# Optimization experiments

Measured on AMD Instinct MI355X. Metric: run time of the kernel, lower is better.

## Reference

```python
import jax, jax.numpy as jnp
import numpy as np

H = 4      # attention heads in HGTConv
DH = 32    # head dim
D = 128    # hidden size (rnn.hidden_size == hidden_size)
PAD = 0    # pad_idx


def setup_inputs() -> dict:
    key = jax.random.key(0)
    ks = jax.random.split(key, 16)
    Na = Np = 50000
    E = 800000
    V = 10000
    L = 8
    s = 0.05  # init scale keeps attention logits stable
    return {
        "tok_author": jax.random.randint(ks[0], (Na, L), 0, V),
        "tok_paper": jax.random.randint(ks[1], (Np, L), 0, V),
        "edge_ap": jax.random.randint(ks[2], (2, E), 0, Np),  # author -> paper
        "edge_pa": jax.random.randint(ks[3], (2, E), 0, Na),  # paper -> author
        "emb": jax.random.normal(ks[4], (V, D)) * s,
        "Wk": jax.random.normal(ks[5], (2, D, D)) * s,
        "Wq": jax.random.normal(ks[6], (2, D, D)) * s,
        "Wv": jax.random.normal(ks[7], (2, D, D)) * s,
        "Watt": jax.random.normal(ks[8], (2, H, DH, DH)) * s,
        "Wmsg": jax.random.normal(ks[9], (2, H, DH, DH)) * s,
        "mu": jnp.ones((2, H), jnp.float32),
        "Wout": jax.random.normal(ks[10], (2, D, D)) * s,
        "lin_w": jax.random.normal(ks[11], (D, D)) * s,
        "lin_b": jnp.zeros((D,), jnp.float32),
    }


def _st_encode(tok, emb):
    # STEncoder stand-in: embedding lookup, pad-masked mean pool, then relu_()
    e = emb[tok]                                   # [N, L, D]
    mask = (tok != PAD).astype(e.dtype)[..., None]  # [N, L, 1]
    pooled = (e * mask).sum(1) / jnp.maximum(mask.sum(1), 1.0)
    return jax.nn.relu(pooled)                     # [N, D]


def _segment_softmax(score, seg, n):
    m = jax.ops.segment_max(score, seg, num_segments=n)
    e = jnp.exp(score - m[seg])
    d = jax.ops.segment_sum(e, seg, num_segments=n)
    return e / (d[seg] + 1e-9)


def _proj(x, W):
    return (x @ W).reshape(x.shape[0], H, DH)


def _rel(k_src, v_src, q_dst, edges, Wa, Wm, mu_r, n_dst):
    # One HGT relation: per-edge key/message transform, segment-softmax attention,
    # scatter-add aggregation into destination nodes.
    src, dst = edges[0], edges[1]
    ke = jnp.einsum('ehd,hdf->ehf', k_src[src], Wa)           # [E, H, DH]
    score = (ke * q_dst[dst]).sum(-1) * mu_r / jnp.sqrt(jnp.float32(DH))  # [E, H]
    alpha = _segment_softmax(score, dst, n_dst)
    me = jnp.einsum('ehd,hdf->ehf', v_src[src], Wm)           # [E, H, DH]
    agg = jax.ops.segment_sum(alpha[..., None] * me, dst, num_segments=n_dst)
    return agg.reshape(n_dst, H * DH)


def reference(tok_author, tok_paper, edge_ap, edge_pa, emb, Wk, Wq, Wv,
              Watt, Wmsg, mu, Wout, lin_w, lin_b):
    # embed + relu per node type
    xa = _st_encode(tok_author, emb)   # [Na, D]
    xp = _st_encode(tok_paper, emb)    # [Np, D]
    Na = xa.shape[0]

    # per-node-type K/Q/V projections (type 0 = author, 1 = paper)
    ka, qa, va = _proj(xa, Wk[0]), _proj(xa, Wq[0]), _proj(xa, Wv[0])
    kp, qp, vp = _proj(xp, Wk[1]), _proj(xp, Wq[1]), _proj(xp, Wv[1])

    # only the 'author' node type feeds the output head, so we only need the
    # paper->author relation's aggregation (rel index 1)
    agg_a = _rel(kp, vp, qa, edge_pa, Watt[1], Wmsg[1], mu[1], Na)
    out_a = jax.nn.gelu(agg_a) @ Wout[0] + xa   # target-type linear + skip

    return out_a @ lin_w + lin_b
```

## Files before the change

kernel.cpp:

```cpp
#include <hip/hip_runtime.h>
#include <math.h>

#define L 8
#define FP8_SCALE 512.0f
#define FP8_INV   0.001953125f

typedef unsigned int  u32;
typedef unsigned short u16;
typedef __attribute__((ext_vector_type(8))) short bf16x8;
typedef __attribute__((ext_vector_type(4))) float f32x4;
typedef __attribute__((ext_vector_type(2))) float f32x2;

__device__ inline u16 f2bf(float x) {
    u32 u = __float_as_uint(x);
    return (u16)((u + 0x7fffu + ((u >> 16) & 1u)) >> 16);
}
__device__ inline float2 bf2f2(u32 v) {
    float2 r;
    r.x = __uint_as_float(v << 16);
    r.y = __uint_as_float(v & 0xffff0000u);
    return r;
}
__device__ inline float gelu_t(float x) {
    return 0.5f * x * (1.0f + tanhf(0.7978845608028654f *
           (x + 0.044715f * x * x * x)));
}

__device__ inline void conv_emb_body(int bid, int tid,
    const float* __restrict__ emb, u32* __restrict__ emb_bf, int n2)
{
    int i = bid * 256 + tid;
    if (i >= n2) return;
    float2 e = *(const float2*)(emb + (size_t)i * 2);
    emb_bf[i] = ((u32)f2bf(e.y) << 16) | (u32)f2bf(e.x);
}

__device__ inline void hist_body8(int bid, int tid,
    const int* __restrict__ dstI, int* __restrict__ deg,
    int* __restrict__ rank, int E, int stride)
{
    int e0 = bid * 256 + tid;
    int d[8], r[8];
#pragma unroll
    for (int j = 0; j < 8; ++j) {
        int e = e0 + j * stride;
        d[j] = (e < E) ? dstI[e] : -1;
    }
#pragma unroll
    for (int j = 0; j < 8; ++j)
        r[j] = (d[j] >= 0) ? atomicAdd(&deg[d[j]], 1) : 0;
#pragma unroll
    for (int j = 0; j < 8; ++j) {
        int e = e0 + j * stride;
        if (d[j] >= 0) rank[e] = r[j];
    }
}

__device__ inline void fold_body(int bid, int tid,
    const float* __restrict__ Wk1, const float* __restrict__ Wq0,
    const float* __restrict__ Wv1, const float* __restrict__ Watt1,
    const float* __restrict__ Wmsg1, const float* __restrict__ Wout0,
    const float* __restrict__ lin_w,
    u16* __restrict__ wkaT, u16* __restrict__ wvmT,
    u16* __restrict__ wqT, u16* __restrict__ w1T, u16* __restrict__ lwT)
{
    int id = bid * 256 + tid;
    int which = id >> 14;
    int idx = id & 16383;
    int col = idx & 127;
    int k = idx >> 7;
    if (which == 0) {
        int h = col >> 5, f = col & 31;
        float s = 0.f;
        for (int d = 0; d < 32; ++d)
            s += Wk1[k * 128 + h * 32 + d] * Watt1[h * 1024 + d * 32 + f];
        wkaT[col * 128 + k] = f2bf(s);
    } else if (which == 1) {
        int h = col >> 5, f = col & 31;
        float s = 0.f;
        for (int d = 0; d < 32; ++d)
            s += Wv1[k * 128 + h * 32 + d] * Wmsg1[h * 1024 + d * 32 + f];
        wvmT[col * 128 + k] = f2bf(s);
    } else if (which == 2) {
        wqT[col * 128 + k] = f2bf(Wq0[k * 128 + col]);
    } else if (which == 3) {
        float s = 0.f;
        for (int d = 0; d < 128; ++d)
            s += Wout0[k * 128 + d] * lin_w[d * 128 + col];
        w1T[col * 128 + k] = f2bf(s);
    } else {
        lwT[col * 128 + k] = f2bf(lin_w[k * 128 + col]);
    }
}

__device__ inline void scan_local_body(int bid, int tid,
    const int* __restrict__ deg, int* __restrict__ locpref,
    int* __restrict__ blocksum, int Na)
{
    __shared__ int lds[256];
    int base = bid * 1024 + tid * 4;
    int4 v = {0, 0, 0, 0};
    if (base + 3 < Na) {
        v = *(const int4*)(deg + base);
    } else {
        if (base + 0 < Na) v.x = deg[base + 0];
        if (base + 1 < Na) v.y = deg[base + 1];
        if (base + 2 < Na) v.z = deg[base + 2];
        if (base + 3 < Na) v.w = deg[base + 3];
    }
    int tot = v.x + v.y + v.z + v.w;
    lds[tid] = tot;
    __syncthreads();
    for (int off = 1; off < 256; off <<= 1) {
        int u = (tid >= off) ? lds[tid - off] : 0;
        __syncthreads();
        lds[tid] += u;
        __syncthreads();
    }
    int excl = lds[tid] - tot;
    if (base < Na) {
        int4 o;
        o.x = excl;
        o.y = excl + v.x;
        o.z = o.y + v.y;
        o.w = o.z + v.z;
        if (base + 3 < Na) *(int4*)(locpref + base) = o;
        else {
            locpref[base] = o.x;
            if (base + 1 < Na) locpref[base + 1] = o.y;
            if (base + 2 < Na) locpref[base + 2] = o.z;
        }
    }
    if (tid == 255) blocksum[bid] = lds[255];
}

__device__ inline void encode_body(int bid, int tid,
    const int* __restrict__ tok_a, const int* __restrict__ tok_p,
    const uint2* __restrict__ emb_bf2,
    uint2* __restrict__ xa2, uint2* __restrict__ xp2, int Na, int Ntot)
{
    int i = bid * 256 + tid;
    int n = i >> 5, q = i & 31;
    if (n >= Ntot) return;
    const int* tok = (n < Na) ? (tok_a + (size_t)n * L)
                              : (tok_p + (size_t)(n - Na) * L);
    int4 t0 = *(const int4*)tok;
    int4 t1 = *(const int4*)(tok + 4);
    int tt[8] = {t0.x, t0.y, t0.z, t0.w, t1.x, t1.y, t1.z, t1.w};
    float ax = 0.f, ay = 0.f, az = 0.f, aw = 0.f;
    int cnt = 0;
#pragma unroll
    for (int l = 0; l < L; ++l) {
        int t = tt[l];
        if (t != 0) {
            cnt++;
            uint2 e = emb_bf2[(size_t)t * 32 + q];
            float2 e0 = bf2f2(e.x), e1 = bf2f2(e.y);
            ax += e0.x; ay += e0.y; az += e1.x; aw += e1.y;
        }
    }
    float dn = 1.0f / fmaxf((float)cnt, 1.0f);
    ax = fmaxf(ax * dn, 0.f); ay = fmaxf(ay * dn, 0.f);
    az = fmaxf(az * dn, 0.f); aw = fmaxf(aw * dn, 0.f);
    uint2 o;
    o.x = ((u32)f2bf(ay) << 16) | (u32)f2bf(ax);
    o.y = ((u32)f2bf(aw) << 16) | (u32)f2bf(az);
    if (n < Na) xa2[(size_t)n * 32 + q] = o;
    else        xp2[(size_t)(n - Na) * 32 + q] = o;
}

__device__ inline void scan_final_body(int bid, int tid,
    const int* __restrict__ locpref, const int* __restrict__ blockoff,
    int* __restrict__ rowptr, int Na)
{
    int i = bid * 256 + tid;
    if (i < Na)
        rowptr[i] = locpref[i] + blockoff[i >> 10];
}

__device__ inline void scatter_body8(int bid, int tid,
    const int* __restrict__ srcI, const int* __restrict__ dstI,
    const int* __restrict__ rank, const int* __restrict__ rowptr,
    int* __restrict__ csrc, int E, int stride)
{
    int e0 = bid * 256 + tid;
    int d[8], s[8], r[8];
#pragma unroll
    for (int j = 0; j < 8; ++j) {
        int e = e0 + j * stride;
        d[j] = (e < E) ? dstI[e] : -1;
        s[j] = (e < E) ? srcI[e] : 0;
        r[j] = (e < E) ? rank[e] : 0;
    }
    int base[8];
#pragma unroll
    for (int j = 0; j < 8; ++j)
        base[j] = (d[j] >= 0) ? rowptr[d[j]] : 0;
#pragma unroll
    for (int j = 0; j < 8; ++j)
        if (d[j] >= 0) csrc[base[j] + r[j]] = s[j];
}

__global__ __launch_bounds__(256) void k_prep(
    const float* emb, u32* emb_bf, int n2,
    const int* dstI, int* deg, int* rank, int E, int Bhist8, int stride,
    const float* Wk1, const float* Wq0, const float* Wv1,
    const float* Watt1, const float* Wmsg1, const float* Wout0,
    const float* lin_w, u16* wkaT, u16* wvmT, u16* wqT, u16* w1T, u16* lwT,
    int Bfold)
{
    int b = blockIdx.x, t = threadIdx.x;
    if (b < Bhist8)               hist_body8(b, t, dstI, deg, rank, E, stride);
    else if (b < Bhist8 + Bfold)  fold_body(b - Bhist8, t, Wk1, Wq0, Wv1,
                                      Watt1, Wmsg1, Wout0, lin_w,
                                      wkaT, wvmT, wqT, w1T, lwT);
    else conv_emb_body(b - Bhist8 - Bfold, t, emb, emb_bf, n2);
}

__global__ __launch_bounds__(256) void k_scan_enc(
    const int* deg, int* locpref, int* blocksum, int Na, int BscanL,
    const int* tok_a, const int* tok_p, const uint2* emb_bf2,
    uint2* xa2, uint2* xp2, int Ntot)
{
    int b = blockIdx.x, t = threadIdx.x;
    if (b < BscanL) scan_local_body(b, t, deg, locpref, blocksum, Na);
    else encode_body(b - BscanL, t, tok_a, tok_p, emb_bf2, xa2, xp2, Na, Ntot);
}

__global__ __launch_bounds__(256) void k_scanb(
    const int* __restrict__ blocksum, int* __restrict__ blockoff,
    int* __restrict__ rowptr, int nb, int Na)
{
    __shared__ int lds[256];
    int t = threadIdx.x;
    int s = (t < nb) ? blocksum[t] : 0;
    lds[t] = s;
    __syncthreads();
    for (int off = 1; off < 256; off <<= 1) {
        int u = (t >= off) ? lds[t - off] : 0;
        __syncthreads();
        lds[t] += u;
        __syncthreads();
    }
    if (t < nb) blockoff[t] = lds[t] - s;
    if (t == 255) rowptr[Na] = lds[255];
}

__global__ __launch_bounds__(256) void k_final(
    const int* locpref, const int* blockoff, int* rowptr, int Na)
{
    scan_final_body(blockIdx.x, threadIdx.x, locpref, blockoff, rowptr, Na);
}

__global__ __launch_bounds__(256) void k_scat_proj(
    const int* srcI, const int* dstI, const int* rank, const int* rowptr,
    int* csrc, int E, int Bscat8, int stride,
    const u16* __restrict__ xa, const u16* __restrict__ xp,
    const u16* __restrict__ wqT, const u16* __restrict__ wkaT,
    const u16* __restrict__ wvmT,
    u16* __restrict__ qa, u32* __restrict__ km8, int Na, int Np, int gba,
    int Bproj)
{
    int b = blockIdx.x, t = threadIdx.x;
    if (b % 3 == 0) {
        int sb = b / 3;
        if (sb < Bscat8)
            scatter_body8(sb, t, srcI, dstI, rank, rowptr, csrc, E, stride);
        return;
    }
    int pb = (b / 3) * 2 + (b % 3 - 1);
    if (pb >= Bproj) return;

    int wave = t >> 6;
    int l = t & 63;
    int x = l & 15;
    int kb = (l >> 4) * 8;

    if (pb < gba) {
        int rbase = pb * 64 + wave * 16;
        int arow = rbase + x;
        if (arow >= Na) arow = Na - 1;
        bf16x8 af[4];
#pragma unroll
        for (int ks = 0; ks < 4; ++ks)
            af[ks] = *(const bf16x8*)(xa + (size_t)arow * 128 + ks * 32 + kb);
        f32x4 acc[8];
#pragma unroll
        for (int ct = 0; ct < 8; ++ct) acc[ct] = (f32x4){0.f, 0.f, 0.f, 0.f};
#pragma unroll
        for (int ks = 0; ks < 4; ++ks)
#pragma unroll
            for (int ct = 0; ct < 8; ++ct) {
                bf16x8 bf = *(const bf16x8*)(wqT + (size_t)(ct * 16 + x) * 128 + ks * 32 + kb);
                acc[ct] = __builtin_amdgcn_mfma_f32_16x16x32_bf16(af[ks], bf, acc[ct], 0, 0, 0);
            }
        int srow = rbase + ((l >> 4) << 2);
#pragma unroll
        for (int ct = 0; ct < 8; ++ct) {
            int col = ct * 16 + x;
#pragma unroll
            for (int r = 0; r < 4; ++r)
                if (srow + r < Na)
                    qa[(size_t)(srow + r) * 128 + col] = f2bf(acc[ct][r]);
        }
    } else {
        int b2 = pb - gba;
        int rbase = b2 * 64 + wave * 16;
        int arow = rbase + x;
        if (arow >= Np) arow = Np - 1;
        bf16x8 af[4];
#pragma unroll
        for (int ks = 0; ks < 4; ++ks)
            af[ks] = *(const bf16x8*)(xp + (size_t)arow * 128 + ks * 32 + kb);
        f32x4 kacc[8], macc[8];
#pragma unroll
        for (int ct = 0; ct < 8; ++ct) {
            kacc[ct] = (f32x4){0.f, 0.f, 0.f, 0.f};
            macc[ct] = (f32x4){0.f, 0.f, 0.f, 0.f};
        }
#pragma unroll
        for (int ks = 0; ks < 4; ++ks)
#pragma unroll
            for (int ct = 0; ct < 8; ++ct) {
                bf16x8 bk = *(const bf16x8*)(wkaT + (size_t)(ct * 16 + x) * 128 + ks * 32 + kb);
                kacc[ct] = __builtin_amdgcn_mfma_f32_16x16x32_bf16(af[ks], bk, kacc[ct], 0, 0, 0);
            }
#pragma unroll
        for (int ks = 0; ks < 4; ++ks)
#pragma unroll
            for (int ct = 0; ct < 8; ++ct) {
                bf16x8 bm = *(const bf16x8*)(wvmT + (size_t)(ct * 16 + x) * 128 + ks * 32 + kb);
                macc[ct] = __builtin_amdgcn_mfma_f32_16x16x32_bf16(af[ks], bm, macc[ct], 0, 0, 0);
            }
        int srow = rbase + ((l >> 4) << 2);
#pragma unroll
        for (int ct = 0; ct < 8; ++ct) {
#pragma unroll
            for (int r = 0; r < 4; ++r) {
                float k0 = kacc[ct][r] * FP8_SCALE;
                float k1 = __shfl_xor(k0, 1);
                float m0 = macc[ct][r] * FP8_SCALE;
                float m1 = __shfl_xor(m0, 1);
                if (!(x & 1) && (srow + r) < Np) {
                    int pk = __builtin_amdgcn_cvt_pk_fp8_f32(k0, k1, 0, false);
                    pk = __builtin_amdgcn_cvt_pk_fp8_f32(m0, m1, pk, true);
                    km8[(size_t)(srow + r) * 64 + ct * 8 + (x >> 1)] = (u32)pk;
                }
            }
        }
    }
}

__device__ inline void e_acc(u32 km, float2 qf, float muh,
                             float& dsum, float& a0, float& a1)
{
    f32x2 kf = __builtin_amdgcn_cvt_pk_f32_fp8(km, false);
    f32x2 mf = __builtin_amdgcn_cvt_pk_f32_fp8(km, true);
    float p = kf.x * qf.x + kf.y * qf.y;
    p += __shfl_xor(p, 1, 16);
    p += __shfl_xor(p, 2, 16);
    p += __shfl_xor(p, 4, 16);
    p += __shfl_xor(p, 8, 16);
    float ev = __expf(p * muh);
    dsum += ev; a0 += ev * mf.x; a1 += ev * mf.y;
}

__global__ __launch_bounds__(256) void csr_agg(
    const u32* __restrict__ km8, const u32* __restrict__ qap,
    const int* __restrict__ rowptr, const int* __restrict__ csrc,
    const float* __restrict__ mu1, u32* __restrict__ gagg, int Na)
{
    int dst = blockIdx.x * 4 + (threadIdx.x >> 6);
    if (dst >= Na) return;
    int lane = threadIdx.x & 63;
    int h = lane >> 4;
    float muh = mu1[h] * 0.17677669529663689f * FP8_INV;
    float2 qf = bf2f2(qap[(size_t)dst * 64 + lane]);

    float a0 = 0.f, a1 = 0.f, dsum = 0.f;
    int beg = rowptr[dst], end = rowptr[dst + 1];

    int i = beg;
    for (; i + 8 <= end; i += 8) {
        int s[8];
        u32 km[8];
#pragma unroll
        for (int j = 0; j < 8; ++j) s[j] = csrc[i + j];
#pragma unroll
        for (int j = 0; j < 8; ++j) km[j] = km8[(size_t)s[j] * 64 + lane];
#pragma unroll
        for (int j = 0; j < 8; ++j) e_acc(km[j], qf, muh, dsum, a0, a1);
    }
    for (; i + 4 <= end; i += 4) {
        int s0 = csrc[i], s1 = csrc[i + 1], s2 = csrc[i + 2], s3 = csrc[i + 3];
        u32 km0 = km8[(size_t)s0 * 64 + lane];
        u32 km1 = km8[(size_t)s1 * 64 + lane];
        u32 km2 = km8[(size_t)s2 * 64 + lane];
        u32 km3 = km8[(size_t)s3 * 64 + lane];
        e_acc(km0, qf, muh, dsum, a0, a1);
        e_acc(km1, qf, muh, dsum, a0, a1);
        e_acc(km2, qf, muh, dsum, a0, a1);
        e_acc(km3, qf, muh, dsum, a0, a1);
    }
    for (; i < end; ++i) {
        u32 km0 = km8[(size_t)csrc[i] * 64 + lane];
        e_acc(km0, qf, muh, dsum, a0, a1);
    }
    float dn = dsum + 1e-9f;
    a0 = gelu_t(a0 / dn * FP8_INV);
    a1 = gelu_t(a1 / dn * FP8_INV);
    gagg[(size_t)dst * 64 + lane] = ((u32)f2bf(a1) << 16) | (u32)f2bf(a0);
}

__global__ __launch_bounds__(256) void mfma_out(
    const u16* __restrict__ A0, const u16* __restrict__ WT0,
    const u16* __restrict__ A1, const u16* __restrict__ WT1,
    const float* __restrict__ bias, float* __restrict__ Y, int N)
{
    int wave = threadIdx.x >> 6;
    int l = threadIdx.x & 63;
    int rbase = blockIdx.x * 64 + wave * 16;
    int arow = rbase + (l & 15);
    if (arow >= N) arow = N - 1;
    int kb = (l >> 4) * 8;

    f32x4 acc[8];
#pragma unroll
    for (int ct = 0; ct < 8; ++ct) acc[ct] = (f32x4){0.f, 0.f, 0.f, 0.f};

    for (int w = 0; w < 2; ++w) {
        const u16* A  = w ? A1 : A0;
        const u16* WT = w ? WT1 : WT0;
        bf16x8 af[4];
#pragma unroll
        for (int ks = 0; ks < 4; ++ks)
            af[ks] = *(const bf16x8*)(A + (size_t)arow * 128 + ks * 32 + kb);
#pragma unroll
        for (int ks = 0; ks < 4; ++ks) {
#pragma unroll
            for (int ct = 0; ct < 8; ++ct) {
                bf16x8 bf = *(const bf16x8*)(WT + (size_t)(ct * 16 + (l & 15)) * 128 + ks * 32 + kb);
                acc[ct] = __builtin_amdgcn_mfma_f32_16x16x32_bf16(af[ks], bf, acc[ct], 0, 0, 0);
            }
        }
    }
    int srow = rbase + ((l >> 4) << 2);
#pragma unroll
    for (int ct = 0; ct < 8; ++ct) {
        int col = ct * 16 + (l & 15);
        float b = bias[col];
#pragma unroll
        for (int r = 0; r < 4; ++r) {
            if (srow + r < N)
                Y[(size_t)(srow + r) * 128 + col] = acc[ct][r] + b;
        }
    }
}

extern "C" void kernel_launch(void* const* d_in, const int* in_sizes, int n_in,
                              void* d_out, int out_size, void* d_ws, size_t ws_size,
                              hipStream_t stream)
{
    const int*   tok_a   = (const int*)d_in[0];
    const int*   tok_p   = (const int*)d_in[1];
    const int*   edge_pa = (const int*)d_in[3];
    const float* emb     = (const float*)d_in[4];
    const float* Wk      = (const float*)d_in[5];
    const float* Wq      = (const float*)d_in[6];
    const float* Wv      = (const float*)d_in[7];
    const float* Watt    = (const float*)d_in[8];
    const float* Wmsg    = (const float*)d_in[9];
    const float* mu      = (const float*)d_in[10];
    const float* Wout    = (const float*)d_in[11];
    const float* lin_w   = (const float*)d_in[12];
    const float* lin_b   = (const float*)d_in[13];

    int Na = in_sizes[0] / L;
    int Np = in_sizes[1] / L;
    int E  = in_sizes[3] / 2;
    int V  = in_sizes[4] / 128;
    float* out = (float*)d_out;

    u16* xa      = (u16*)d_ws;
    u16* qa      = xa + (size_t)Na * 128;
    u16* xp      = qa + (size_t)Na * 128;
    u16* gagg    = xp + (size_t)Np * 128;
    u16* emb_bf  = gagg + (size_t)Na * 128;
    u32* km8     = (u32*)(emb_bf + (size_t)V * 128);
    int* deg     = (int*)(km8 + (size_t)Np * 64);
    int* locpref = deg + Na;
    int* rowptr  = locpref + Na;
    int* csrc    = rowptr + Na + 2;
    int* blocksum= csrc + E;
    int* blockoff= blocksum + 256;
    u16* wkaT    = (u16*)(blockoff + 256);
    u16* wvmT    = wkaT + 16384;
    u16* wqT     = wvmT + 16384;
    u16* w1T     = wqT + 16384;
    u16* lwT     = w1T + 16384;
    int* rank    = (int*)gagg;

    const int* e_src = edge_pa;
    const int* e_dst = edge_pa + E;

    int n2emb  = V * 64;
    int Bconv  = (n2emb + 255) / 256;
    int Bfold  = (5 * 16384) / 256;
    int Bhist8 = (E + 2047) / 2048;
    int hstride = Bhist8 * 256;
    int nb     = (Na + 1023) / 1024;
    int Ntot   = Na + Np;
    int Benc   = ((size_t)Ntot * 32 + 255) / 256;
    int BscanF = (Na + 255) / 256;
    int gba    = (Na + 63) / 64;
    int gbp    = (Np + 63) / 64;
    int Bproj  = gba + gbp;
    int Bscat8 = (E + 2047) / 2048;
    int sstride = Bscat8 * 256;

    (void)hipMemsetAsync(deg, 0, (size_t)Na * sizeof(int), stream);

    k_prep<<<Bhist8 + Bfold + Bconv, 256, 0, stream>>>(
        emb, (u32*)emb_bf, n2emb,
        e_dst, deg, rank, E, Bhist8, hstride,
        Wk + 16384, Wq, Wv + 16384, Watt + 4096, Wmsg + 4096, Wout, lin_w,
        wkaT, wvmT, wqT, w1T, lwT, Bfold);

    k_scan_enc<<<nb + Benc, 256, 0, stream>>>(
        deg, locpref, blocksum, Na, nb,
        tok_a, tok_p, (const uint2*)emb_bf, (uint2*)xa, (uint2*)xp, Ntot);

    k_scanb<<<1, 256, 0, stream>>>(blocksum, blockoff, rowptr, nb, Na);

    k_final<<<BscanF, 256, 0, stream>>>(locpref, blockoff, rowptr, Na);

    int Gunit = (Bscat8 > (Bproj + 1) / 2) ? Bscat8 : (Bproj + 1) / 2;
    k_scat_proj<<<3 * Gunit, 256, 0, stream>>>(
        e_src, e_dst, rank, rowptr, csrc, E, Bscat8, sstride,
        xa, xp, wqT, wkaT, wvmT, qa, km8, Na, Np, gba, Bproj);

    csr_agg<<<(Na + 3) / 4, 256, 0, stream>>>(
        km8, (const u32*)qa, rowptr, csrc, mu + 4, (u32*)gagg, Na);

    mfma_out<<<gba, 256, 0, stream>>>(gagg, w1T, xa, lwT, lin_b, out, Na);
}
```

Baseline: 213.1 us.

## Fuse scan kernels, move skip-path GEMM into projection kernel, widen scatter unroll

Merges the single-block block-offset scan into the final rowptr kernel, with every block redoing the small 256-entry scan in LDS, which removes one launch. The skip-path GEMM (xa @ lin_w + bias) moves into the combined scatter/projection kernel so it runs alongside other work. The last kernel then only adds gagg @ W1 into out with a read-modify-write. The edge scatter processes 16 edges per thread instead of 8. The trade-offs are extra fp32 output traffic from the read-modify-write, redundant scan work in each block, and higher register pressure in the scatter.

```diff
diff --git a/kernel.cpp b/kernel.cpp
--- a/kernel.cpp
+++ b/kernel.cpp
@@ -169,35 +169,26 @@
     else        xp2[(size_t)(n - Na) * 32 + q] = o;
 }
 
-__device__ inline void scan_final_body(int bid, int tid,
-    const int* __restrict__ locpref, const int* __restrict__ blockoff,
-    int* __restrict__ rowptr, int Na)
-{
-    int i = bid * 256 + tid;
-    if (i < Na)
-        rowptr[i] = locpref[i] + blockoff[i >> 10];
-}
-
-__device__ inline void scatter_body8(int bid, int tid,
+__device__ inline void scatter_body16(int bid, int tid,
     const int* __restrict__ srcI, const int* __restrict__ dstI,
     const int* __restrict__ rank, const int* __restrict__ rowptr,
     int* __restrict__ csrc, int E, int stride)
 {
     int e0 = bid * 256 + tid;
-    int d[8], s[8], r[8];
-#pragma unroll
-    for (int j = 0; j < 8; ++j) {
+    int d[16], s[16], r[16];
+#pragma unroll
+    for (int j = 0; j < 16; ++j) {
         int e = e0 + j * stride;
         d[j] = (e < E) ? dstI[e] : -1;
         s[j] = (e < E) ? srcI[e] : 0;
         r[j] = (e < E) ? rank[e] : 0;
     }
-    int base[8];
-#pragma unroll
-    for (int j = 0; j < 8; ++j)
+    int base[16];
+#pragma unroll
+    for (int j = 0; j < 16; ++j)
         base[j] = (d[j] >= 0) ? rowptr[d[j]] : 0;
 #pragma unroll
-    for (int j = 0; j < 8; ++j)
+    for (int j = 0; j < 16; ++j)
         if (d[j] >= 0) csrc[base[j] + r[j]] = s[j];
 }
 
@@ -227,11 +218,12 @@
     else encode_body(b - BscanL, t, tok_a, tok_p, emb_bf2, xa2, xp2, Na, Ntot);
 }
 
-__global__ __launch_bounds__(256) void k_scanb(
-    const int* __restrict__ blocksum, int* __restrict__ blockoff,
+__global__ __launch_bounds__(256) void k_final(
+    const int* __restrict__ locpref, const int* __restrict__ blocksum,
     int* __restrict__ rowptr, int nb, int Na)
 {
     __shared__ int lds[256];
+    __shared__ int excl[256];
     int t = threadIdx.x;
     int s = (t < nb) ? blocksum[t] : 0;
     lds[t] = s;
@@ -242,30 +234,30 @@
         lds[t] += u;
         __syncthreads();
     }
-    if (t < nb) blockoff[t] = lds[t] - s;
-    if (t == 255) rowptr[Na] = lds[255];
-}
-
-__global__ __launch_bounds__(256) void k_final(
-    const int* locpref, const int* blockoff, int* rowptr, int Na)
-{
-    scan_final_body(blockIdx.x, threadIdx.x, locpref, blockoff, rowptr, Na);
+    excl[t] = lds[t] - s;
+    __syncthreads();
+    int i = blockIdx.x * 256 + t;
+    if (i < Na)
+        rowptr[i] = locpref[i] + excl[i >> 10];
+    if (blockIdx.x == 0 && t == 0)
+        rowptr[Na] = lds[nb - 1];
 }
 
 __global__ __launch_bounds__(256) void k_scat_proj(
     const int* srcI, const int* dstI, const int* rank, const int* rowptr,
-    int* csrc, int E, int Bscat8, int stride,
+    int* csrc, int E, int Bscat16, int stride,
     const u16* __restrict__ xa, const u16* __restrict__ xp,
     const u16* __restrict__ wqT, const u16* __restrict__ wkaT,
-    const u16* __restrict__ wvmT,
-    u16* __restrict__ qa, u32* __restrict__ km8, int Na, int Np, int gba,
-    int Bproj)
+    const u16* __restrict__ wvmT, const u16* __restrict__ lwT,
+    const float* __restrict__ lin_b,
+    u16* __restrict__ qa, u32* __restrict__ km8, float* __restrict__ outp,
+    int Na, int Np, int gba, int gbp, int Bproj)
 {
     int b = blockIdx.x, t = threadIdx.x;
     if (b % 3 == 0) {
         int sb = b / 3;
-        if (sb < Bscat8)
-            scatter_body8(sb, t, srcI, dstI, rank, rowptr, csrc, E, stride);
+        if (sb < Bscat16)
+            scatter_body16(sb, t, srcI, dstI, rank, rowptr, csrc, E, stride);
         return;
     }
     int pb = (b / 3) * 2 + (b % 3 - 1);
@@ -303,7 +295,7 @@
                 if (srow + r < Na)
                     qa[(size_t)(srow + r) * 128 + col] = f2bf(acc[ct][r]);
         }
-    } else {
+    } else if (pb < gba + gbp) {
         int b2 = pb - gba;
         int rbase = b2 * 64 + wave * 16;
         int arow = rbase + x;
@@ -348,6 +340,35 @@
                 }
             }
         }
+    } else {
+        int b3 = pb - gba - gbp;
+        int rbase = b3 * 64 + wave * 16;
+        int arow = rbase + x;
+        if (arow >= Na) arow = Na - 1;
+        bf16x8 af[4];
+#pragma unroll
+        for (int ks = 0; ks < 4; ++ks)
+            af[ks] = *(const bf16x8*)(xa + (size_t)arow * 128 + ks * 32 + kb);
+        f32x4 acc[8];
+#pragma unroll
+        for (int ct = 0; ct < 8; ++ct) acc[ct] = (f32x4){0.f, 0.f, 0.f, 0.f};
+#pragma unroll
+        for (int ks = 0; ks < 4; ++ks)
+#pragma unroll
+            for (int ct = 0; ct < 8; ++ct) {
+                bf16x8 bf = *(const bf16x8*)(lwT + (size_t)(ct * 16 + x) * 128 + ks * 32 + kb);
+                acc[ct] = __builtin_amdgcn_mfma_f32_16x16x32_bf16(af[ks], bf, acc[ct], 0, 0, 0);
+            }
+        int srow = rbase + ((l >> 4) << 2);
+#pragma unroll
+        for (int ct = 0; ct < 8; ++ct) {
+            int col = ct * 16 + x;
+            float bb = lin_b[col];
+#pragma unroll
+            for (int r = 0; r < 4; ++r)
+                if (srow + r < Na)
+                    outp[(size_t)(srow + r) * 128 + col] = acc[ct][r] + bb;
+        }
     }
 }
 
@@ -412,10 +433,9 @@
     gagg[(size_t)dst * 64 + lane] = ((u32)f2bf(a1) << 16) | (u32)f2bf(a0);
 }
 
-__global__ __launch_bounds__(256) void mfma_out(
+__global__ __launch_bounds__(256) void mfma_acc(
     const u16* __restrict__ A0, const u16* __restrict__ WT0,
-    const u16* __restrict__ A1, const u16* __restrict__ WT1,
-    const float* __restrict__ bias, float* __restrict__ Y, int N)
+    float* __restrict__ Y, int N)
 {
     int wave = threadIdx.x >> 6;
     int l = threadIdx.x & 63;
@@ -424,35 +444,32 @@
     if (arow >= N) arow = N - 1;
     int kb = (l >> 4) * 8;
 
+    bf16x8 af[4];
+#pragma unroll
+    for (int ks = 0; ks < 4; ++ks)
+        af[ks] = *(const bf16x8*)(A0 + (size_t)arow * 128 + ks * 32 + kb);
+
     f32x4 acc[8];
 #pragma unroll
     for (int ct = 0; ct < 8; ++ct) acc[ct] = (f32x4){0.f, 0.f, 0.f, 0.f};
-
-    for (int w = 0; w < 2; ++w) {
-        const u16* A  = w ? A1 : A0;
-        const u16* WT = w ? WT1 : WT0;
-        bf16x8 af[4];
-#pragma unroll
-        for (int ks = 0; ks < 4; ++ks)
-            af[ks] = *(const bf16x8*)(A + (size_t)arow * 128 + ks * 32 + kb);
-#pragma unroll
-        for (int ks = 0; ks < 4; ++ks) {
-#pragma unroll
-            for (int ct = 0; ct < 8; ++ct) {
-                bf16x8 bf = *(const bf16x8*)(WT + (size_t)(ct * 16 + (l & 15)) * 128 + ks * 32 + kb);
-                acc[ct] = __builtin_amdgcn_mfma_f32_16x16x32_bf16(af[ks], bf, acc[ct], 0, 0, 0);
-            }
-        }
-    }
+#pragma unroll
+    for (int ks = 0; ks < 4; ++ks)
+#pragma unroll
+        for (int ct = 0; ct < 8; ++ct) {
+            bf16x8 bf = *(const bf16x8*)(WT0 + (size_t)(ct * 16 + (l & 15)) * 128 + ks * 32 + kb);
+            acc[ct] = __builtin_amdgcn_mfma_f32_16x16x32_bf16(af[ks], bf, acc[ct], 0, 0, 0);
+        }
+
     int srow = rbase + ((l >> 4) << 2);
 #pragma unroll
     for (int ct = 0; ct < 8; ++ct) {
         int col = ct * 16 + (l & 15);
-        float b = bias[col];
 #pragma unroll
         for (int r = 0; r < 4; ++r) {
-            if (srow + r < N)
-                Y[(size_t)(srow + r) * 128 + col] = acc[ct][r] + b;
+            if (srow + r < N) {
+                size_t o = (size_t)(srow + r) * 128 + col;
+                Y[o] += acc[ct][r];
+            }
         }
     }
 }
@@ -492,8 +509,7 @@
     int* rowptr  = locpref + Na;
     int* csrc    = rowptr + Na + 2;
     int* blocksum= csrc + E;
-    int* blockoff= blocksum + 256;
-    u16* wkaT    = (u16*)(blockoff + 256);
+    u16* wkaT    = (u16*)(blocksum + 256);
     u16* wvmT    = wkaT + 16384;
     u16* wqT     = wvmT + 16384;
     u16* w1T     = wqT + 16384;
@@ -503,20 +519,20 @@
     const int* e_src = edge_pa;
     const int* e_dst = edge_pa + E;
 
-    int n2emb  = V * 64;
-    int Bconv  = (n2emb + 255) / 256;
-    int Bfold  = (5 * 16384) / 256;
-    int Bhist8 = (E + 2047) / 2048;
+    int n2emb   = V * 64;
+    int Bconv   = (n2emb + 255) / 256;
+    int Bfold   = (5 * 16384) / 256;
+    int Bhist8  = (E + 2047) / 2048;
     int hstride = Bhist8 * 256;
-    int nb     = (Na + 1023) / 1024;
-    int Ntot   = Na + Np;
-    int Benc   = ((size_t)Ntot * 32 + 255) / 256;
-    int BscanF = (Na + 255) / 256;
-    int gba    = (Na + 63) / 64;
-    int gbp    = (Np + 63) / 64;
-    int Bproj  = gba + gbp;
-    int Bscat8 = (E + 2047) / 2048;
-    int sstride = Bscat8 * 256;
+    int nb      = (Na + 1023) / 1024;
+    int Ntot    = Na + Np;
+    int Benc    = ((size_t)Ntot * 32 + 255) / 256;
+    int BscanF  = (Na + 255) / 256;
+    int gba     = (Na + 63) / 64;
+    int gbp     = (Np + 63) / 64;
+    int Bproj   = gba + gbp + gba;
+    int Bscat16 = (E + 4095) / 4096;
+    int sstride = Bscat16 * 256;
 
     (void)hipMemsetAsync(deg, 0, (size_t)Na * sizeof(int), stream);
 
@@ -530,17 +546,16 @@
         deg, locpref, blocksum, Na, nb,
         tok_a, tok_p, (const uint2*)emb_bf, (uint2*)xa, (uint2*)xp, Ntot);
 
-    k_scanb<<<1, 256, 0, stream>>>(blocksum, blockoff, rowptr, nb, Na);
-
-    k_final<<<BscanF, 256, 0, stream>>>(locpref, blockoff, rowptr, Na);
-
-    int Gunit = (Bscat8 > (Bproj + 1) / 2) ? Bscat8 : (Bproj + 1) / 2;
+    k_final<<<BscanF, 256, 0, stream>>>(locpref, blocksum, rowptr, nb, Na);
+
+    int Gunit = (Bscat16 > (Bproj + 1) / 2) ? Bscat16 : (Bproj + 1) / 2;
     k_scat_proj<<<3 * Gunit, 256, 0, stream>>>(
-        e_src, e_dst, rank, rowptr, csrc, E, Bscat8, sstride,
-        xa, xp, wqT, wkaT, wvmT, qa, km8, Na, Np, gba, Bproj);
+        e_src, e_dst, rank, rowptr, csrc, E, Bscat16, sstride,
+        xa, xp, wqT, wkaT, wvmT, lwT, lin_b,
+        qa, km8, out, Na, Np, gba, gbp, Bproj);
 
     csr_agg<<<(Na + 3) / 4, 256, 0, stream>>>(
         km8, (const u32*)qa, rowptr, csrc, mu + 4, (u32*)gagg, Na);
 
-    mfma_out<<<gba, 256, 0, stream>>>(gagg, w1T, xa, lwT, lin_b, out, Na);
-}
+    mfma_acc<<<gba, 256, 0, stream>>>(gagg, w1T, out, Na);
+}
```

Result: slower. 220.8 us (+3.6%).
